# Kernel optimization log

Hardware: AMD Instinct MI355X
Metric: run time of the kernel (lower is better)

Reference implementation:

```python
import jax, jax.numpy as jnp
import numpy as np

B, H, K, V = 32, 32, 256, 256
CLIP = 1e6


def setup_inputs() -> dict:
    key = jax.random.key(0)
    k1, k2, k3, k4, k5 = jax.random.split(key, 5)
    state = jax.random.normal(k1, (B, H, K, V), dtype=jnp.float32)
    keys = jax.random.normal(k2, (B, H, K), dtype=jnp.float32)
    values = jax.random.normal(k3, (B, H, V), dtype=jnp.float32)
    gates = jax.random.uniform(k4, (B, H, K), dtype=jnp.float32)  # forget gates alpha in (0,1)
    beta = jax.random.uniform(k5, (B, H, 1), dtype=jnp.float32)   # learning rate beta in (0,1)
    return {"state": state, "keys": keys, "values": values, "gates": gates, "beta": beta}


def reference(state, keys, values, gates, beta):
    # KDA delta-rule update: S_t = (I - beta k k^T) Diag(alpha) S_{t-1} + beta k v^T
    state_decayed = gates[..., None] * state                       # (B,H,K,V)
    kt_state = jnp.einsum('bhk,bhkv->bhv', keys, state_decayed)    # k^T (Diag(a) S)
    beta_e = beta[..., None]                                       # (B,H,1,1)
    correction = beta_e * jnp.einsum('bhk,bhv->bhkv', keys, kt_state)
    kv_update = beta_e * jnp.einsum('bhk,bhv->bhkv', keys, values)
    new_state = state_decayed - correction + kv_update
    # NaN -> revert to previous state; Inf -> clip (matches torch module's checks)
    has_nan = jnp.isnan(new_state).any()
    has_inf = jnp.isinf(new_state).any()
    new_state = jnp.where(has_nan, state,
                          jnp.where(has_inf, jnp.clip(new_state, -CLIP, CLIP), new_state))
    return new_state
```

## Files before the change

kernel.cpp:

```cpp
#include <hip/hip_runtime.h>


#define KD 256
#define VD 256
#define VD4 (VD / 4)

typedef float f32x4 __attribute__((ext_vector_type(4)));

__global__ __launch_bounds__(256, 2)
void kda_update_kernel(const float* __restrict__ state,
                       const float* __restrict__ keys,
                       const float* __restrict__ values,
                       const float* __restrict__ gates,
                       const float* __restrict__ beta,
                       float* __restrict__ out)
{
    const int bid  = blockIdx.x;
    const int bh   = bid >> 1;
    const int half = bid & 1;
    const size_t toff = (size_t)bh * (KD * VD);
    const f32x4* __restrict__ S4 = (const f32x4*)(state + toff);
    f32x4* __restrict__ O4 = (f32x4*)(out + toff);

    __shared__ float s_g[KD];
    __shared__ float s_w[KD];
    __shared__ float s_c[KD];

    const int t    = threadIdx.x;
    const int wv   = t >> 6;
    const int lane = t & 63;
    const int r8   = lane >> 3;
    const int c8   = lane & 7;
    const int col  = half * 32 + wv * 8 + c8;

    {
        const float g = gates[bh * KD + t];
        const float k = keys[bh * KD + t];
        s_g[t] = g;
        s_w[t] = g * k;
        s_c[t] = beta[bh] * k;
    }
    __syncthreads();

    f32x4 s[32];
#pragma unroll
    for (int j = 0; j < 32; ++j)
        s[j] = __builtin_nontemporal_load(&S4[(size_t)(r8 + 8 * j) * VD4 + col]);

    f32x4 p = (f32x4)(0.f);
#pragma unroll
    for (int j = 0; j < 32; ++j) {
        const float w = s_w[r8 + 8 * j];
        p.x = fmaf(w, s[j].x, p.x);
        p.y = fmaf(w, s[j].y, p.y);
        p.z = fmaf(w, s[j].z, p.z);
        p.w = fmaf(w, s[j].w, p.w);
    }

#pragma unroll
    for (int m = 8; m <= 32; m <<= 1) {
        p.x += __shfl_xor(p.x, m, 64);
        p.y += __shfl_xor(p.y, m, 64);
        p.z += __shfl_xor(p.z, m, 64);
        p.w += __shfl_xor(p.w, m, 64);
    }

    const f32x4 vv = ((const f32x4*)(values + (size_t)bh * VD))[col];
    f32x4 d;
    d.x = vv.x - p.x; d.y = vv.y - p.y;
    d.z = vv.z - p.z; d.w = vv.w - p.w;

#pragma unroll
    for (int j = 0; j < 32; ++j) {
        const int r = r8 + 8 * j;
        const float g  = s_g[r];
        const float cb = s_c[r];
        f32x4 o;
        o.x = fmaf(g, s[j].x, cb * d.x);
        o.y = fmaf(g, s[j].y, cb * d.y);
        o.z = fmaf(g, s[j].z, cb * d.z);
        o.w = fmaf(g, s[j].w, cb * d.w);
        __builtin_nontemporal_store(o, &O4[(size_t)r * VD4 + col]);
    }
}

extern "C" void kernel_launch(void* const* d_in, const int* in_sizes, int n_in,
                              void* d_out, int out_size, void* d_ws, size_t ws_size,
                              hipStream_t stream) {
    const float* state  = (const float*)d_in[0];
    const float* keys   = (const float*)d_in[1];
    const float* values = (const float*)d_in[2];
    const float* gates  = (const float*)d_in[3];
    const float* beta   = (const float*)d_in[4];
    float* out = (float*)d_out;

    dim3 grid(32 * 32 * 2);
    dim3 block(256);
    hipLaunchKernelGGL(kda_update_kernel, grid, block, 0, stream,
                       state, keys, values, gates, beta, out);
}
```

Measured before the change: 97.12 us.

## Split each head across 8 column-group blocks with cross-wave LDS reduction

Work decomposition changes from 2 blocks of 256 threads per (b,h) to 8 blocks of 128 threads. Each block now covers 8 float4 columns, and its two waves each take half of the K rows. The partial k^T S sums from the two waves are combined through a small LDS buffer and an extra barrier. The barrier now uses a raw s_waitcnt plus s_barrier instead of __syncthreads. The intent is to halve per-thread register state, raise occupancy and give a finer grid for better latency hiding, at the cost of more blocks, an extra sync, and gate/key loads repeated by more blocks.

After: 113.7 us. +17.1%, slower.

```diff
diff --git a/kernel.cpp b/kernel.cpp
--- a/kernel.cpp
+++ b/kernel.cpp
@@ -7,7 +7,12 @@
 
 typedef float f32x4 __attribute__((ext_vector_type(4)));
 
-__global__ __launch_bounds__(256, 2)
+__device__ __forceinline__ void lds_barrier() {
+    asm volatile("s_waitcnt lgkmcnt(0)" ::: "memory");
+    __builtin_amdgcn_s_barrier();
+}
+
+__global__ __launch_bounds__(128, 4)
 void kda_update_kernel(const float* __restrict__ state,
                        const float* __restrict__ keys,
                        const float* __restrict__ values,
@@ -15,9 +20,9 @@
                        const float* __restrict__ beta,
                        float* __restrict__ out)
 {
-    const int bid  = blockIdx.x;
-    const int bh   = bid >> 1;
-    const int half = bid & 1;
+    const int bid = blockIdx.x;
+    const int bh  = bid >> 3;
+    const int cg  = bid & 7;
     const size_t toff = (size_t)bh * (KD * VD);
     const f32x4* __restrict__ S4 = (const f32x4*)(state + toff);
     f32x4* __restrict__ O4 = (f32x4*)(out + toff);
@@ -25,32 +30,36 @@
     __shared__ float s_g[KD];
     __shared__ float s_w[KD];
     __shared__ float s_c[KD];
+    __shared__ f32x4 s_x[2][8];
 
     const int t    = threadIdx.x;
     const int wv   = t >> 6;
     const int lane = t & 63;
     const int r8   = lane >> 3;
     const int c8   = lane & 7;
-    const int col  = half * 32 + wv * 8 + c8;
+    const int col  = cg * 8 + c8;
+    const int rbase = wv * 128;
 
-    {
-        const float g = gates[bh * KD + t];
-        const float k = keys[bh * KD + t];
-        s_g[t] = g;
-        s_w[t] = g * k;
-        s_c[t] = beta[bh] * k;
+#pragma unroll
+    for (int i = 0; i < 2; ++i) {
+        const int r = t + 128 * i;
+        const float g = gates[bh * KD + r];
+        const float k = keys[bh * KD + r];
+        s_g[r] = g;
+        s_w[r] = g * k;
+        s_c[r] = beta[bh] * k;
     }
-    __syncthreads();
+    lds_barrier();
 
-    f32x4 s[32];
+    f32x4 s[16];
 #pragma unroll
-    for (int j = 0; j < 32; ++j)
-        s[j] = __builtin_nontemporal_load(&S4[(size_t)(r8 + 8 * j) * VD4 + col]);
+    for (int j = 0; j < 16; ++j)
+        s[j] = __builtin_nontemporal_load(&S4[(size_t)(rbase + r8 + 8 * j) * VD4 + col]);
 
     f32x4 p = (f32x4)(0.f);
 #pragma unroll
-    for (int j = 0; j < 32; ++j) {
-        const float w = s_w[r8 + 8 * j];
+    for (int j = 0; j < 16; ++j) {
+        const float w = s_w[rbase + r8 + 8 * j];
         p.x = fmaf(w, s[j].x, p.x);
         p.y = fmaf(w, s[j].y, p.y);
         p.z = fmaf(w, s[j].z, p.z);
@@ -65,14 +74,21 @@
         p.w += __shfl_xor(p.w, m, 64);
     }
 
+    if (lane < 8) s_x[wv][lane] = p;
+    lds_barrier();
+    {
+        const f32x4 q = s_x[wv ^ 1][c8];
+        p.x += q.x; p.y += q.y; p.z += q.z; p.w += q.w;
+    }
+
     const f32x4 vv = ((const f32x4*)(values + (size_t)bh * VD))[col];
     f32x4 d;
     d.x = vv.x - p.x; d.y = vv.y - p.y;
     d.z = vv.z - p.z; d.w = vv.w - p.w;
 
 #pragma unroll
-    for (int j = 0; j < 32; ++j) {
-        const int r = r8 + 8 * j;
+    for (int j = 0; j < 16; ++j) {
+        const int r = rbase + r8 + 8 * j;
         const float g  = s_g[r];
         const float cb = s_c[r];
         f32x4 o;
@@ -94,8 +110,8 @@
     const float* beta   = (const float*)d_in[4];
     float* out = (float*)d_out;
 
-    dim3 grid(32 * 32 * 2);
-    dim3 block(256);
+    dim3 grid(32 * 32 * 8);
+    dim3 block(128);
     hipLaunchKernelGGL(kda_update_kernel, grid, block, 0, stream,
                        state, keys, values, gates, beta, out);
 }
```
